# Optimization experiments

Hardware: AMD Instinct MI355X
Metric: run time of the kernel (lower is better)

Reference implementation:

```python
import jax, jax.numpy as jnp
import numpy as np

BOUND = 2.0
CASCADE = 2            # 1 + ceil(log2(bound))
GRID = 128             # self.gridSize
MIN_NEAR = 0.05        # args.minNear
DENSITY_THRESH = 10.0  # args.densityThresh
MAX_STEPS = 128        # args.maxSteps
BLOB_DENSITY = 5.0     # args.blobDensity
BLOB_RADIUS = 0.2      # args.blobRadius
N_RAYS = 131072


def near_far_from_aabb(o, d, bound, min_near):
    # slab method against the cube [-bound, bound]^3
    inv = 1.0 / jnp.where(jnp.abs(d) > 1e-8, d, 1e-8)
    t0 = (-bound - o) * inv
    t1 = (bound - o) * inv
    tmin = jnp.max(jnp.minimum(t0, t1), axis=-1)
    tmax = jnp.min(jnp.maximum(t0, t1), axis=-1)
    near = jnp.maximum(tmin, min_near)
    far = jnp.maximum(tmax, near + 1e-6)
    return near, far


def query_sigma(xyz, density_grid):
    # cascade selection: cas = ceil(log2(max|xyz|)) clamped to [0, CASCADE)
    mx = jnp.max(jnp.abs(xyz), axis=-1)
    cas = jnp.clip(jnp.ceil(jnp.log2(jnp.maximum(mx, 1.0))), 0, CASCADE - 1).astype(jnp.int32)
    bound_c = jnp.exp2(cas.astype(xyz.dtype))[..., None]
    u = jnp.clip(xyz / bound_c * 0.5 + 0.5, 0.0, 1.0 - 1e-6)
    idx = (u * GRID).astype(jnp.int32)  # [N,3] voxel coords
    occ = density_grid[cas, idx[..., 0], idx[..., 1], idx[..., 2]] > DENSITY_THRESH
    # density field stand-in: the module's densityBlob with 'exp' activation
    d2 = jnp.sum(xyz * xyz, axis=-1)
    sigma = BLOB_DENSITY * jnp.exp(-d2 / (2.0 * BLOB_RADIUS ** 2))
    return jnp.where(occ, sigma, 0.0)


def setup_inputs() -> dict:
    key = jax.random.key(0)
    k1, k2, k3 = jax.random.split(key, 3)
    # camera cluster slightly outside the volume, looking toward the origin
    raysO = jax.random.normal(k1, (N_RAYS, 3), dtype=jnp.float32) * 0.1 + jnp.array([0.0, 0.0, 2.5], jnp.float32)
    d = jax.random.normal(k2, (N_RAYS, 3), dtype=jnp.float32)
    d = d.at[:, 2].add(-3.0)
    raysD = d / jnp.linalg.norm(d, axis=-1, keepdims=True)
    densityGrid = jax.random.uniform(k3, (CASCADE, GRID, GRID, GRID), dtype=jnp.float32) * 30.0
    return {"raysO": raysO, "raysD": raysD, "densityGrid": densityGrid}


def reference(raysO, raysD, densityGrid):
    near, far = near_far_from_aabb(raysO, raysD, BOUND, MIN_NEAR)
    dt = (far - near) / MAX_STEPS  # [N] per-ray step size
    N = raysO.shape[0]

    def step(carry, i):
        T, image, depth, wsum = carry
        t = near + (i.astype(near.dtype) + 0.5) * dt          # [N]
        xyz = raysO + t[:, None] * raysD                       # [N,3]
        sigma = query_sigma(xyz, densityGrid)                  # [N]
        alpha = 1.0 - jnp.exp(-sigma * dt)
        w = alpha * T                                          # weights
        rgb = jnp.clip(xyz / (2.0 * BOUND) + 0.5, 0.0, 1.0)    # rgb stand-in (albedo)
        image = image + w[:, None] * rgb
        depth = depth + w * t
        wsum = wsum + w
        T = T * (1.0 - alpha)                                  # transmittance update
        return (T, image, depth, wsum), None

    init = (jnp.ones(N, jnp.float32), jnp.zeros((N, 3), jnp.float32),
            jnp.zeros(N, jnp.float32), jnp.zeros(N, jnp.float32))
    (T, image, depth, wsum), _ = jax.lax.scan(step, init, jnp.arange(MAX_STEPS))
    # background composite: image + (1 - weightsSum) * bgColor with bgColor = 1
    image = image + (1.0 - wsum)[:, None] * 1.0
    return image
```

## Files before the change

kernel.cpp:

```cpp
#include <hip/hip_runtime.h>

#define N_RAYS     131072
#define MAX_STEPS  128
#define R2_CULL    0.65f

__device__ __forceinline__ float opq(float x) { asm("" : "+v"(x)); return x; }

__global__ __launch_bounds__(256) void renderer_kernel(
    const float* __restrict__ raysO,
    const float* __restrict__ raysD,
    const float* __restrict__ grid,
    float* __restrict__ out)
{
    #pragma clang fp contract(off)

    const int tid = blockIdx.x * blockDim.x + threadIdx.x;
    const int r   = tid >> 2;
    const int seg = tid & 3;
    if (r >= N_RAYS) return;

    const float ox = raysO[3*r+0], oy = raysO[3*r+1], oz = raysO[3*r+2];
    const float dx = raysD[3*r+0], dy = raysD[3*r+1], dz = raysD[3*r+2];

    const float sdx = (fabsf(dx) > 1e-8f) ? dx : 1e-8f;
    const float sdy = (fabsf(dy) > 1e-8f) ? dy : 1e-8f;
    const float sdz = (fabsf(dz) > 1e-8f) ? dz : 1e-8f;
    const float rdx = opq(1.0f / sdx);
    const float rdy = opq(1.0f / sdy);
    const float rdz = opq(1.0f / sdz);
    const float t0x = opq(opq(-2.0f - ox) * rdx);
    const float t1x = opq(opq( 2.0f - ox) * rdx);
    const float t0y = opq(opq(-2.0f - oy) * rdy);
    const float t1y = opq(opq( 2.0f - oy) * rdy);
    const float t0z = opq(opq(-2.0f - oz) * rdz);
    const float t1z = opq(opq( 2.0f - oz) * rdz);
    const float tmin = fmaxf(fmaxf(fminf(t0x, t1x), fminf(t0y, t1y)), fminf(t0z, t1z));
    const float tmax = fminf(fminf(fmaxf(t0x, t1x), fmaxf(t0y, t1y)), fmaxf(t0z, t1z));
    const float nearT = fmaxf(tmin, 0.05f);
    const float farT  = fmaxf(tmax, opq(nearT + 1e-6f));
    const float dtv   = opq(opq(farT - nearT) * 0.0078125f);

    int s_lo = 0, s_hi = -1;
    {
        const float b    = ox*dx + oy*dy + oz*dz;
        const float c    = ox*ox + oy*oy + oz*oz - R2_CULL;
        const float disc = b*b - c;
        if (disc > 0.0f) {
            const float sq = sqrtf(disc) + 0.01f;
            const float inv_dt = 1.0f / dtv;
            float fs_lo = (-b - sq - nearT) * inv_dt - 0.5f;
            float fs_hi = (-b + sq - nearT) * inv_dt - 0.5f;
            fs_lo = fminf(fmaxf(fs_lo, -2.0f), 130.0f);
            fs_hi = fminf(fmaxf(fs_hi, -2.0f), 130.0f);
            s_lo = max(0, (int)floorf(fs_lo) - 1);
            s_hi = min(MAX_STEPS - 1, (int)ceilf(fs_hi) + 1);
        }
    }

    float T = 1.0f;
    float accR = 0.0f, accG = 0.0f, accB = 0.0f;
    float wsum = 0.0f;

    const float INV_2R2 = 1.0f / 0.08f;

    const int n = s_hi - s_lo + 1;
    if (n > 0) {
        const int per = (n + 3) >> 2;
        const int lo  = s_lo + seg * per;
        const int hi  = min(lo + per - 1, s_hi);

        #pragma unroll 8
        for (int s = lo; s <= hi; ++s) {
            const float sp = opq((float)s + 0.5f);
            const float t  = opq(__builtin_fmaf(sp, dtv, nearT));
            const float x  = opq(ox + opq(t * dx));
            const float y  = opq(oy + opq(t * dy));
            const float z  = opq(oz + opq(t * dz));

            const float ux = opq(opq(x * 0.5f) + 0.5f);
            const float uy = opq(opq(y * 0.5f) + 0.5f);
            const float uz = opq(opq(z * 0.5f) + 0.5f);
            const int ixv = (int)opq(ux * 128.0f);
            const int iyv = (int)opq(uy * 128.0f);
            const int izv = (int)opq(uz * 128.0f);

            const int gi = (ixv << 14) + (iyv << 7) + izv;
            const bool occ = grid[gi] > 10.0f;

            const float d2     = __builtin_fmaf(x, x, __builtin_fmaf(y, y, z * z));
            const float sigma0 = 5.0f * __expf(-(d2 * INV_2R2));
            const float sigma  = occ ? sigma0 : 0.0f;
            const float alpha  = 1.0f - __expf(-(sigma * dtv));
            const float w      = alpha * T;

            const float cr = __builtin_fmaf(x, 0.25f, 0.5f);
            const float cg = __builtin_fmaf(y, 0.25f, 0.5f);
            const float cb = __builtin_fmaf(z, 0.25f, 0.5f);

            accR = __builtin_fmaf(w, cr, accR);
            accG = __builtin_fmaf(w, cg, accG);
            accB = __builtin_fmaf(w, cb, accB);
            wsum += w;
            T *= (1.0f - alpha);
        }
    }

    const int lane = threadIdx.x & 63;
    #pragma unroll
    for (int m = 1; m <= 2; m <<= 1) {
        const float To  = __shfl_xor(T,    m);
        const float aRo = __shfl_xor(accR, m);
        const float aGo = __shfl_xor(accG, m);
        const float aBo = __shfl_xor(accB, m);
        const float wo  = __shfl_xor(wsum, m);
        const bool left = ((lane & m) == 0);
        const float Tf  = left ? T    : To;
        const float aR1 = left ? accR : aRo, aR2 = left ? aRo : accR;
        const float aG1 = left ? accG : aGo, aG2 = left ? aGo : accG;
        const float aB1 = left ? accB : aBo, aB2 = left ? aBo : accB;
        const float w1  = left ? wsum : wo,  w2  = left ? wo  : wsum;
        accR = aR1 + Tf * aR2;
        accG = aG1 + Tf * aG2;
        accB = aB1 + Tf * aB2;
        wsum = w1  + Tf * w2;
        T    = T * To;
    }

    if (seg == 0) {
        const float bg = 1.0f - wsum;
        out[3*r+0] = accR + bg;
        out[3*r+1] = accG + bg;
        out[3*r+2] = accB + bg;
    }
}

extern "C" void kernel_launch(void* const* d_in, const int* in_sizes, int n_in,
                              void* d_out, int out_size, void* d_ws, size_t ws_size,
                              hipStream_t stream) {
    const float* raysO = (const float*)d_in[0];
    const float* raysD = (const float*)d_in[1];
    const float* grid  = (const float*)d_in[2];
    float* out = (float*)d_out;

    const int threads = 256;
    const int total   = N_RAYS * 4;
    const int blocks  = (total + threads - 1) / threads;
    renderer_kernel<<<blocks, threads, 0, stream>>>(raysO, raysD, grid, out);
}
```

Measured before the change: 18.42 us.

## Split each ray across 16 lanes with per-chunk shuffle-scan compositing

Each ray is now handled by 16 threads instead of 4. The lanes process consecutive steps in chunks of 16, and each chunk is combined with a 4-level xor-shuffle scan of transmittance and colour before folding into a running accumulator. Launch bounds now request 8 blocks per CU. The aim is more parallelism and shorter per-thread serial loops. In exchange it launches four times as many threads, repeats the ray setup in every lane, and pays shuffle overhead on every chunk.

```diff
diff --git a/kernel.cpp b/kernel.cpp
--- a/kernel.cpp
+++ b/kernel.cpp
@@ -6,7 +6,7 @@
 
 __device__ __forceinline__ float opq(float x) { asm("" : "+v"(x)); return x; }
 
-__global__ __launch_bounds__(256) void renderer_kernel(
+__global__ __launch_bounds__(256, 8) void renderer_kernel(
     const float* __restrict__ raysO,
     const float* __restrict__ raysD,
     const float* __restrict__ grid,
@@ -14,9 +14,9 @@
 {
     #pragma clang fp contract(off)
 
-    const int tid = blockIdx.x * blockDim.x + threadIdx.x;
-    const int r   = tid >> 2;
-    const int seg = tid & 3;
+    const int tid  = blockIdx.x * blockDim.x + threadIdx.x;
+    const int r    = tid >> 4;
+    const int lane16 = tid & 15;
     if (r >= N_RAYS) return;
 
     const float ox = raysO[3*r+0], oy = raysO[3*r+1], oz = raysO[3*r+2];
@@ -57,76 +57,73 @@
         }
     }
 
-    float T = 1.0f;
+    float Trun = 1.0f;
     float accR = 0.0f, accG = 0.0f, accB = 0.0f;
     float wsum = 0.0f;
 
     const float INV_2R2 = 1.0f / 0.08f;
 
-    const int n = s_hi - s_lo + 1;
-    if (n > 0) {
-        const int per = (n + 3) >> 2;
-        const int lo  = s_lo + seg * per;
-        const int hi  = min(lo + per - 1, s_hi);
+    for (int base = s_lo; base <= s_hi; base += 16) {
+        const int  s_raw = base + lane16;
+        const bool valid = (s_raw <= s_hi);
+        const int  s     = min(s_raw, s_hi);
 
-        #pragma unroll 8
-        for (int s = lo; s <= hi; ++s) {
-            const float sp = opq((float)s + 0.5f);
-            const float t  = opq(__builtin_fmaf(sp, dtv, nearT));
-            const float x  = opq(ox + opq(t * dx));
-            const float y  = opq(oy + opq(t * dy));
-            const float z  = opq(oz + opq(t * dz));
+        const float sp = opq((float)s + 0.5f);
+        const float t  = opq(__builtin_fmaf(sp, dtv, nearT));
+        const float x  = opq(ox + opq(t * dx));
+        const float y  = opq(oy + opq(t * dy));
+        const float z  = opq(oz + opq(t * dz));
 
-            const float ux = opq(opq(x * 0.5f) + 0.5f);
-            const float uy = opq(opq(y * 0.5f) + 0.5f);
-            const float uz = opq(opq(z * 0.5f) + 0.5f);
-            const int ixv = (int)opq(ux * 128.0f);
-            const int iyv = (int)opq(uy * 128.0f);
-            const int izv = (int)opq(uz * 128.0f);
+        const float ux = opq(opq(x * 0.5f) + 0.5f);
+        const float uy = opq(opq(y * 0.5f) + 0.5f);
+        const float uz = opq(opq(z * 0.5f) + 0.5f);
+        const int ixv = (int)opq(ux * 128.0f);
+        const int iyv = (int)opq(uy * 128.0f);
+        const int izv = (int)opq(uz * 128.0f);
 
-            const int gi = (ixv << 14) + (iyv << 7) + izv;
-            const bool occ = grid[gi] > 10.0f;
+        const float gv = grid[(ixv << 14) + (iyv << 7) + izv];
+        const bool occ = valid && (gv > 10.0f);
 
-            const float d2     = __builtin_fmaf(x, x, __builtin_fmaf(y, y, z * z));
-            const float sigma0 = 5.0f * __expf(-(d2 * INV_2R2));
-            const float sigma  = occ ? sigma0 : 0.0f;
-            const float alpha  = 1.0f - __expf(-(sigma * dtv));
-            const float w      = alpha * T;
+        const float d2     = __builtin_fmaf(x, x, __builtin_fmaf(y, y, z * z));
+        const float sigma0 = 5.0f * __expf(-(d2 * INV_2R2));
+        const float sigma  = occ ? sigma0 : 0.0f;
+        const float alpha  = 1.0f - __expf(-(sigma * dtv));
 
-            const float cr = __builtin_fmaf(x, 0.25f, 0.5f);
-            const float cg = __builtin_fmaf(y, 0.25f, 0.5f);
-            const float cb = __builtin_fmaf(z, 0.25f, 0.5f);
+        float Tl  = 1.0f - alpha;
+        float aRl = alpha * __builtin_fmaf(x, 0.25f, 0.5f);
+        float aGl = alpha * __builtin_fmaf(y, 0.25f, 0.5f);
+        float aBl = alpha * __builtin_fmaf(z, 0.25f, 0.5f);
+        float wl  = alpha;
 
-            accR = __builtin_fmaf(w, cr, accR);
-            accG = __builtin_fmaf(w, cg, accG);
-            accB = __builtin_fmaf(w, cb, accB);
-            wsum += w;
-            T *= (1.0f - alpha);
+        const int lane = threadIdx.x & 63;
+        #pragma unroll
+        for (int m = 1; m <= 8; m <<= 1) {
+            const float To  = __shfl_xor(Tl,  m);
+            const float aRo = __shfl_xor(aRl, m);
+            const float aGo = __shfl_xor(aGl, m);
+            const float aBo = __shfl_xor(aBl, m);
+            const float wo  = __shfl_xor(wl,  m);
+            const bool left = ((lane & m) == 0);
+            const float Tf  = left ? Tl  : To;
+            const float aR1 = left ? aRl : aRo, aR2 = left ? aRo : aRl;
+            const float aG1 = left ? aGl : aGo, aG2 = left ? aGo : aGl;
+            const float aB1 = left ? aBl : aBo, aB2 = left ? aBo : aBl;
+            const float w1  = left ? wl  : wo,  w2  = left ? wo  : wl;
+            aRl = aR1 + Tf * aR2;
+            aGl = aG1 + Tf * aG2;
+            aBl = aB1 + Tf * aB2;
+            wl  = w1  + Tf * w2;
+            Tl  = Tl * To;
         }
+
+        accR = accR + Trun * aRl;
+        accG = accG + Trun * aGl;
+        accB = accB + Trun * aBl;
+        wsum = wsum + Trun * wl;
+        Trun = Trun * Tl;
     }
 
-    const int lane = threadIdx.x & 63;
-    #pragma unroll
-    for (int m = 1; m <= 2; m <<= 1) {
-        const float To  = __shfl_xor(T,    m);
-        const float aRo = __shfl_xor(accR, m);
-        const float aGo = __shfl_xor(accG, m);
-        const float aBo = __shfl_xor(accB, m);
-        const float wo  = __shfl_xor(wsum, m);
-        const bool left = ((lane & m) == 0);
-        const float Tf  = left ? T    : To;
-        const float aR1 = left ? accR : aRo, aR2 = left ? aRo : accR;
-        const float aG1 = left ? accG : aGo, aG2 = left ? aGo : accG;
-        const float aB1 = left ? accB : aBo, aB2 = left ? aBo : accB;
-        const float w1  = left ? wsum : wo,  w2  = left ? wo  : wsum;
-        accR = aR1 + Tf * aR2;
-        accG = aG1 + Tf * aG2;
-        accB = aB1 + Tf * aB2;
-        wsum = w1  + Tf * w2;
-        T    = T * To;
-    }
-
-    if (seg == 0) {
+    if (lane16 == 0) {
         const float bg = 1.0f - wsum;
         out[3*r+0] = accR + bg;
         out[3*r+1] = accG + bg;
@@ -143,7 +140,7 @@
     float* out = (float*)d_out;
 
     const int threads = 256;
-    const int total   = N_RAYS * 4;
-    const int blocks  = (total + threads - 1) / threads;
+    const long long total = (long long)N_RAYS * 16;
+    const int blocks  = (int)((total + threads - 1) / threads);
     renderer_kernel<<<blocks, threads, 0, stream>>>(raysO, raysD, grid, out);
 }
```

Measured after the change: 31.92 us. 1.73x slower.
